# Performance work log

Hardware: AMD Instinct MI355X
Metric: run time of the kernel (lower is better)

## Reference

```python
import jax, jax.numpy as jnp
import numpy as np

B, S, D = 8, 2048, 1024  # batch, seq_len, emb_dim == qkv_dim
NEG = -999999.0  # module uses -999999 instead of -inf


def setup_inputs() -> dict:
    key = jax.random.key(0)
    ks = jax.random.split(key, 4)
    inputs = jax.random.normal(ks[0], (B, S, D), dtype=jnp.float32)
    # causal mask, flax attention layout [B, 1, S, S]
    causal = jnp.tril(jnp.ones((S, S), dtype=bool))
    mask = jnp.broadcast_to(causal, (B, 1, S, S))
    scale = 1.0 / np.sqrt(D)
    Wq = jax.random.normal(ks[1], (D, D), dtype=jnp.float32) * scale
    Wk = jax.random.normal(ks[2], (D, D), dtype=jnp.float32) * scale
    Wv = jax.random.normal(ks[3], (D, D), dtype=jnp.float32) * scale
    z = jnp.zeros((D,), dtype=jnp.float32)
    return {"inputs": inputs, "mask": mask, "Wq": Wq, "bq": z, "Wk": Wk,
            "bk": z, "Wv": Wv, "bv": z}


def reference(inputs, mask, Wq, bq, Wk, bk, Wv, bv):
    q = inputs @ Wq + bq  # [B,S,D]
    k = inputs @ Wk + bk
    v = inputs @ Wv + bv
    depth = q.shape[-1]
    q = q / jnp.sqrt(jnp.asarray(depth, q.dtype))
    attn = jnp.einsum('bqd,bkd->bqk', q, k)  # [B,S,S]
    attn = jnp.where(jnp.squeeze(mask, axis=1), attn, NEG)
    attn = jax.nn.softmax(attn, axis=-1)
    return attn @ v  # [B,S,D]
```

## Files before the change

### kernel.cpp

```cpp
#include <hip/hip_runtime.h>
#include <hip/hip_bf16.h>
#include <cstdint>

#define S_LEN 2048
#define D_DIM 1024
#define NB 8

typedef __attribute__((ext_vector_type(8))) short bf16x8;
typedef __attribute__((ext_vector_type(4))) float f32x4;

__device__ __forceinline__ unsigned short f2bf(float f) {
  union { float f; unsigned u; } x; x.f = f;
  unsigned r = x.u + 0x7fffu + ((x.u >> 16) & 1u);
  return (unsigned short)(r >> 16);
}
__device__ __forceinline__ void gload16(const void* g, void* l) {
  __builtin_amdgcn_global_load_lds((const __attribute__((address_space(1))) void*)g,
                                   (__attribute__((address_space(3))) void*)l, 16, 0, 0);
}

__global__ __launch_bounds__(256)
void cvt_f32_bf16(const float* __restrict__ in, unsigned short* __restrict__ out, int n4) {
  int i = blockIdx.x * blockDim.x + threadIdx.x;
  if (i >= n4) return;
  float4 v = reinterpret_cast<const float4*>(in)[i];
  ushort4 o;
  o.x = f2bf(v.x); o.y = f2bf(v.y); o.z = f2bf(v.z); o.w = f2bf(v.w);
  reinterpret_cast<ushort4*>(out)[i] = o;
}

__global__ __launch_bounds__(256)
void transpose_f32_bf16(const float* __restrict__ in, unsigned short* __restrict__ out,
                        int rows, int cols) {
  __shared__ unsigned short tile[32][33];
  int bx = blockIdx.x * 32, by = blockIdx.y * 32;
  int tx = threadIdx.x, ty = threadIdx.y;
  #pragma unroll
  for (int i = ty; i < 32; i += 8)
    tile[i][tx] = f2bf(in[(size_t)(by + i) * cols + bx + tx]);
  __syncthreads();
  #pragma unroll
  for (int i = ty; i < 32; i += 8)
    out[(size_t)(bx + i) * rows + by + tx] = tile[tx][i];
}

__global__ __launch_bounds__(256)
void transpose_bf16(const unsigned short* __restrict__ in, unsigned short* __restrict__ out,
                    int ldin, int ldout, long zin, long zout) {
  __shared__ unsigned short tile[32][33];
  const unsigned short* ip = in + (size_t)blockIdx.z * zin;
  unsigned short* op = out + (size_t)blockIdx.z * zout;
  int bx = blockIdx.x * 32, by = blockIdx.y * 32;
  int tx = threadIdx.x, ty = threadIdx.y;
  #pragma unroll
  for (int i = ty; i < 32; i += 8)
    tile[i][tx] = ip[(size_t)(by + i) * ldin + bx + tx];
  __syncthreads();
  #pragma unroll
  for (int i = ty; i < 32; i += 8)
    op[(size_t)(bx + i) * ldout + by + tx] = tile[tx][i];
}

#define LDFRAG(S, BUF, MH)                                                        \
  { _Pragma("unroll") for (int i_ = 0; i_ < 4; ++i_)                              \
      af##S[i_] = *reinterpret_cast<const bf16x8*>(&As[BUF][offA[(MH)*4+i_]]);    \
    _Pragma("unroll") for (int i_ = 0; i_ < 4; ++i_)                              \
      bf##S[i_] = *reinterpret_cast<const bf16x8*>(&Bs[BUF][offB[i_]]); }

#define DOMFMA(S, MH)                                                             \
  { __builtin_amdgcn_s_setprio(1);                                                \
    _Pragma("unroll") for (int i_ = 0; i_ < 4; ++i_)                              \
      _Pragma("unroll") for (int j_ = 0; j_ < 4; ++j_)                            \
        acc[(MH)*4+i_][j_] = __builtin_amdgcn_mfma_f32_16x16x32_bf16(             \
            af##S[i_], bf##S[j_], acc[(MH)*4+i_][j_], 0, 0, 0);                   \
    __builtin_amdgcn_s_setprio(0); }

template<int MODE>
__global__ __launch_bounds__(512, 2)
void gemm8(const unsigned short* __restrict__ Aall, const unsigned short* __restrict__ Btall,
           void* __restrict__ Call, int Kd, int lda, int ldb, int ldc,
           long sAz, long sBz, long sCz,
           const float* __restrict__ b0, const float* __restrict__ b1,
           const float* __restrict__ b2, float* __restrict__ rowsum, int ntn) {
  __shared__ __align__(16) unsigned short As[4][8192];
  __shared__ __align__(16) unsigned short Bs[4][8192];
  int nwg = gridDim.x, bid = blockIdx.x;
  int wg = (bid & 7) * (nwg >> 3) + (bid >> 3);
  int tm = wg / ntn, tn = wg % ntn;
  int z = blockIdx.z;
  if (MODE == 1 && tn > tm) return;
  const unsigned short* A  = Aall  + (size_t)z * sAz;
  const unsigned short* Bt = Btall + (size_t)z * sBz;
  int m0 = tm * 256, n0 = tn * 256;
  int t = threadIdx.x, lane = t & 63, w = t >> 6;
  int wr = w >> 2, wc = w & 3;
  int lr = lane & 15, lq = lane >> 4;
  int nkt = (MODE == 2) ? (tm + 1) * 8 : (Kd >> 5);

  int offA[8], offB[4];
  #pragma unroll
  for (int mi = 0; mi < 8; ++mi) {
    int row = wr * 128 + mi * 16 + lr;
    offA[mi] = row * 32 + ((lq ^ ((row >> 1) & 3)) * 8);
  }
  #pragma unroll
  for (int ni = 0; ni < 4; ++ni) {
    int row = wc * 64 + ni * 16 + lr;
    offB[ni] = row * 32 + ((lq ^ ((row >> 1) & 3)) * 8);
  }
  int srow[2], soff[2];
  #pragma unroll
  for (int c = 0; c < 2; ++c) {
    int r = c * 128 + w * 16 + (lane >> 2);
    srow[c] = r;
    soff[c] = ((lane & 3) ^ ((r >> 1) & 3)) * 8;
  }

  f32x4 acc[8][4];
  f32x4 zero4 = {0.f, 0.f, 0.f, 0.f};
  #pragma unroll
  for (int mi = 0; mi < 8; ++mi)
    #pragma unroll
    for (int ni = 0; ni < 4; ++ni) acc[mi][ni] = zero4;

  auto stgA = [&](int buf, int kt2) {
    int kb = kt2 * 32;
    #pragma unroll
    for (int c = 0; c < 2; ++c)
      gload16(A + (size_t)(m0 + srow[c]) * lda + kb + soff[c], &As[buf][c * 4096 + w * 512]);
  };
  auto stgB = [&](int buf, int kt2) {
    int kb = kt2 * 32;
    #pragma unroll
    for (int c = 0; c < 2; ++c)
      gload16(Bt + (size_t)(n0 + srow[c]) * ldb + kb + soff[c], &Bs[buf][c * 4096 + w * 512]);
  };

  stgA(0, 0); stgB(0, 0); stgA(1, 1); stgB(1, 1); stgA(2, 2); stgB(2, 2);
  asm volatile("s_waitcnt vmcnt(8)" ::: "memory");
  __builtin_amdgcn_s_barrier();
  __builtin_amdgcn_sched_barrier(0);
  bf16x8 af0[4], bf0[4], af1[4], bf1[4];
  LDFRAG(0, 0, 0);

  for (int kt = 0; kt < nkt; ++kt) {
    int bcur = kt & 3, bpre = (kt + 3) & 3, bnxt = (kt + 1) & 3;
    bool stg = (kt + 3 < nkt);
    if (stg) stgA(bpre, kt + 3);
    LDFRAG(1, bcur, 1);
    asm volatile("s_waitcnt lgkmcnt(8)" ::: "memory");
    __builtin_amdgcn_sched_barrier(0);
    DOMFMA(0, 0);
    if (stg) stgB(bpre, kt + 3);
    if (kt + 1 < nkt) {
      if (kt <= nkt - 4)      asm volatile("s_waitcnt vmcnt(8)" ::: "memory");
      else if (kt == nkt - 3) asm volatile("s_waitcnt vmcnt(4)" ::: "memory");
      else                    asm volatile("s_waitcnt vmcnt(0)" ::: "memory");
      __builtin_amdgcn_s_barrier();
      __builtin_amdgcn_sched_barrier(0);
      LDFRAG(0, bnxt, 0);
      asm volatile("s_waitcnt lgkmcnt(8)" ::: "memory");
    } else {
      asm volatile("s_waitcnt lgkmcnt(0)" ::: "memory");
    }
    __builtin_amdgcn_sched_barrier(0);
    DOMFMA(1, 1);
  }
  __syncthreads();

  unsigned short* ep = &As[0][0] + w * 4096;
  int lq4 = lq << 4;

  if (MODE == 0) {
    unsigned short* C = (unsigned short*)Call;
    #pragma unroll
    for (int mh = 0; mh < 2; ++mh) {
      #pragma unroll
      for (int mi2 = 0; mi2 < 4; ++mi2)
        #pragma unroll
        for (int ni = 0; ni < 4; ++ni) {
          int col = ni * 16 + lr;
          int gcol = n0 + wc * 64 + col;
          float bb, sc;
          if (gcol < 1024)      { bb = b0[gcol];        sc = 0.03125f; }
          else if (gcol < 2048) { bb = b1[gcol - 1024]; sc = 1.0f; }
          else                  { bb = b2[gcol - 2048]; sc = 1.0f; }
          #pragma unroll
          for (int j = 0; j < 4; ++j) {
            int lrow = mi2 * 16 + lq * 4 + j;
            ep[lrow * 64 + (col ^ lq4)] = f2bf((acc[mh * 4 + mi2][ni][j] + bb) * sc);
          }
        }
      #pragma unroll
      for (int pass = 0; pass < 8; ++pass) {
        int rrow = pass * 8 + (lane >> 3);
        int c8 = (lane & 7) * 8;
        int sw = ((rrow >> 2) & 3) << 4;
        bf16x8 vv = *reinterpret_cast<const bf16x8*>(&ep[rrow * 64 + (c8 ^ sw)]);
        int grow = m0 + wr * 128 + mh * 64 + rrow;
        *reinterpret_cast<bf16x8*>(&C[(size_t)grow * ldc + n0 + wc * 64 + c8]) = vv;
      }
      asm volatile("s_waitcnt lgkmcnt(0)" ::: "memory");
    }
  } else if (MODE == 1) {
    unsigned short* C = (unsigned short*)Call + (size_t)z * sCz;
    float* rs = rowsum + z * S_LEN;
    #pragma unroll
    for (int mh = 0; mh < 2; ++mh) {
      #pragma unroll
      for (int mi2 = 0; mi2 < 4; ++mi2)
        #pragma unroll
        for (int j = 0; j < 4; ++j) {
          int lrow = mi2 * 16 + lq * 4 + j;
          int grow = m0 + wr * 128 + mh * 64 + lrow;
          float partial = 0.f;
          #pragma unroll
          for (int ni = 0; ni < 4; ++ni) {
            int col = ni * 16 + lr;
            int gcol = n0 + wc * 64 + col;
            float e = (gcol <= grow) ? __expf(acc[mh * 4 + mi2][ni][j]) : 0.f;
            partial += e;
            ep[lrow * 64 + (col ^ lq4)] = f2bf(e);
          }
          #pragma unroll
          for (int off = 1; off < 16; off <<= 1) partial += __shfl_xor(partial, off);
          if (lr == 0) atomicAdd(&rs[grow], partial);
        }
      #pragma unroll
      for (int pass = 0; pass < 8; ++pass) {
        int rrow = pass * 8 + (lane >> 3);
        int c8 = (lane & 7) * 8;
        int sw = ((rrow >> 2) & 3) << 4;
        bf16x8 vv = *reinterpret_cast<const bf16x8*>(&ep[rrow * 64 + (c8 ^ sw)]);
        int grow = m0 + wr * 128 + mh * 64 + rrow;
        *reinterpret_cast<bf16x8*>(&C[(size_t)grow * ldc + n0 + wc * 64 + c8]) = vv;
      }
      asm volatile("s_waitcnt lgkmcnt(0)" ::: "memory");
    }
  } else {
    float* C = (float*)Call + (size_t)z * sCz;
    const float* rs = rowsum + z * S_LEN;
    #pragma unroll
    for (int mi = 0; mi < 8; ++mi)
      #pragma unroll
      for (int j = 0; j < 4; ++j) {
        int row = m0 + wr * 128 + mi * 16 + lq * 4 + j;
        float inv = 1.f / rs[row];
        #pragma unroll
        for (int ni = 0; ni < 4; ++ni) {
          int col = n0 + wc * 64 + ni * 16 + lr;
          C[(size_t)row * ldc + col] = acc[mi][ni][j] * inv;
        }
      }
  }
}

extern "C" void kernel_launch(void* const* d_in, const int* in_sizes, int n_in,
                              void* d_out, int out_size, void* d_ws, size_t ws_size,
                              hipStream_t stream) {
  (void)in_sizes; (void)n_in; (void)out_size; (void)ws_size;
  const float* X  = (const float*)d_in[0];
  const float* Wq = (const float*)d_in[2];
  const float* bq = (const float*)d_in[3];
  const float* Wk = (const float*)d_in[4];
  const float* bk = (const float*)d_in[5];
  const float* Wv = (const float*)d_in[6];
  const float* bv = (const float*)d_in[7];

  char* ws = (char*)d_ws;
  unsigned short* Xb  = (unsigned short*)(ws);
  unsigned short* Wt  = (unsigned short*)(ws + 33554432L);
  float*          Rs  = (float*)(ws + 33554432L);
  unsigned short* QKV = (unsigned short*)(ws + 39845888L);
  unsigned short* Pb  = (unsigned short*)(ws + 140509184L);
  unsigned short* Vt  = Xb;

  cvt_f32_bf16<<<16384, 256, 0, stream>>>(X, Xb, (NB * S_LEN * D_DIM) / 4);
  dim3 tb(32, 8);
  transpose_f32_bf16<<<dim3(32, 32), tb, 0, stream>>>(Wq, Wt + 0L * 1048576L, D_DIM, D_DIM);
  transpose_f32_bf16<<<dim3(32, 32), tb, 0, stream>>>(Wk, Wt + 1L * 1048576L, D_DIM, D_DIM);
  transpose_f32_bf16<<<dim3(32, 32), tb, 0, stream>>>(Wv, Wt + 2L * 1048576L, D_DIM, D_DIM);
  gemm8<0><<<dim3(64 * 12, 1, 1), 512, 0, stream>>>(Xb, Wt, (void*)QKV,
      D_DIM, D_DIM, D_DIM, 3 * D_DIM,
      0L, 0L, 0L, bq, bk, bv, nullptr, 12);
  hipMemsetAsync(Rs, 0, NB * S_LEN * sizeof(float), stream);
  gemm8<1><<<dim3(64, 1, NB), 512, 0, stream>>>(QKV, QKV + 1024, (void*)Pb,
      D_DIM, 3 * D_DIM, 3 * D_DIM, S_LEN,
      (long)S_LEN * 3 * D_DIM, (long)S_LEN * 3 * D_DIM, (long)S_LEN * S_LEN,
      nullptr, nullptr, nullptr, Rs, 8);
  transpose_bf16<<<dim3(32, 64, NB), tb, 0, stream>>>(QKV + 2048, Vt,
      3 * D_DIM, S_LEN, (long)S_LEN * 3 * D_DIM, (long)D_DIM * S_LEN);
  gemm8<2><<<dim3(32, 1, NB), 512, 0, stream>>>(Pb, Vt, d_out,
      S_LEN, S_LEN, S_LEN, D_DIM,
      (long)S_LEN * S_LEN, (long)D_DIM * S_LEN, (long)S_LEN * D_DIM,
      nullptr, nullptr, nullptr, Rs, 4);
}
```

Baseline: 340.1 us.

## Restructure GEMM main loop to two-stage prefetch with barrier-interleaved MFMA phases

Replaces the 3-deep global-to-LDS prefetch, which double-buffered register fragments across iterations, with a 2-deep prefetch. Each iteration now loads its A/B fragments, runs half the MFMAs, loads the second A half, and runs the other half. Extra s_barriers around each MFMA phase are meant to keep waves in lockstep, ping-ponging between memory and compute. The trade-off is that it drops the cross-iteration overlap of LDS reads with MFMAs and adds barriers. The shallower prefetch may also expose global-load latency.

```diff
diff --git a/kernel.cpp b/kernel.cpp
--- a/kernel.cpp
+++ b/kernel.cpp
@@ -60,20 +60,6 @@
   for (int i = ty; i < 32; i += 8)
     op[(size_t)(bx + i) * ldout + by + tx] = tile[tx][i];
 }
-
-#define LDFRAG(S, BUF, MH)                                                        \
-  { _Pragma("unroll") for (int i_ = 0; i_ < 4; ++i_)                              \
-      af##S[i_] = *reinterpret_cast<const bf16x8*>(&As[BUF][offA[(MH)*4+i_]]);    \
-    _Pragma("unroll") for (int i_ = 0; i_ < 4; ++i_)                              \
-      bf##S[i_] = *reinterpret_cast<const bf16x8*>(&Bs[BUF][offB[i_]]); }
-
-#define DOMFMA(S, MH)                                                             \
-  { __builtin_amdgcn_s_setprio(1);                                                \
-    _Pragma("unroll") for (int i_ = 0; i_ < 4; ++i_)                              \
-      _Pragma("unroll") for (int j_ = 0; j_ < 4; ++j_)                            \
-        acc[(MH)*4+i_][j_] = __builtin_amdgcn_mfma_f32_16x16x32_bf16(             \
-            af##S[i_], bf##S[j_], acc[(MH)*4+i_][j_], 0, 0, 0);                   \
-    __builtin_amdgcn_s_setprio(0); }
 
 template<int MODE>
 __global__ __launch_bounds__(512, 2)
@@ -136,35 +122,50 @@
       gload16(Bt + (size_t)(n0 + srow[c]) * ldb + kb + soff[c], &Bs[buf][c * 4096 + w * 512]);
   };
 
-  stgA(0, 0); stgB(0, 0); stgA(1, 1); stgB(1, 1); stgA(2, 2); stgB(2, 2);
-  asm volatile("s_waitcnt vmcnt(8)" ::: "memory");
+  stgA(0, 0); stgB(0, 0); stgA(1, 1); stgB(1, 1);
+  asm volatile("s_waitcnt vmcnt(4)" ::: "memory");
   __builtin_amdgcn_s_barrier();
-  __builtin_amdgcn_sched_barrier(0);
-  bf16x8 af0[4], bf0[4], af1[4], bf1[4];
-  LDFRAG(0, 0, 0);
 
   for (int kt = 0; kt < nkt; ++kt) {
-    int bcur = kt & 3, bpre = (kt + 3) & 3, bnxt = (kt + 1) & 3;
-    bool stg = (kt + 3 < nkt);
-    if (stg) stgA(bpre, kt + 3);
-    LDFRAG(1, bcur, 1);
-    asm volatile("s_waitcnt lgkmcnt(8)" ::: "memory");
+    const int bcur = kt & 3, bpre = (kt + 2) & 3;
+    const bool stg = (kt + 2 < nkt);
+    const unsigned short* Ac = &As[bcur][0];
+    const unsigned short* Bc = &Bs[bcur][0];
+    bf16x8 af[4], bfv[4];
+
+    #pragma unroll
+    for (int i = 0; i < 4; ++i) af[i]  = *reinterpret_cast<const bf16x8*>(&Ac[offA[i]]);
+    #pragma unroll
+    for (int i = 0; i < 4; ++i) bfv[i] = *reinterpret_cast<const bf16x8*>(&Bc[offB[i]]);
+    if (stg) stgA(bpre, kt + 2);
+    __builtin_amdgcn_s_barrier();
+    asm volatile("s_waitcnt lgkmcnt(0)" ::: "memory");
     __builtin_amdgcn_sched_barrier(0);
-    DOMFMA(0, 0);
-    if (stg) stgB(bpre, kt + 3);
-    if (kt + 1 < nkt) {
-      if (kt <= nkt - 4)      asm volatile("s_waitcnt vmcnt(8)" ::: "memory");
-      else if (kt == nkt - 3) asm volatile("s_waitcnt vmcnt(4)" ::: "memory");
-      else                    asm volatile("s_waitcnt vmcnt(0)" ::: "memory");
-      __builtin_amdgcn_s_barrier();
-      __builtin_amdgcn_sched_barrier(0);
-      LDFRAG(0, bnxt, 0);
-      asm volatile("s_waitcnt lgkmcnt(8)" ::: "memory");
-    } else {
-      asm volatile("s_waitcnt lgkmcnt(0)" ::: "memory");
-    }
+    __builtin_amdgcn_s_setprio(1);
+    #pragma unroll
+    for (int i = 0; i < 4; ++i)
+      #pragma unroll
+      for (int j = 0; j < 4; ++j)
+        acc[i][j] = __builtin_amdgcn_mfma_f32_16x16x32_bf16(af[i], bfv[j], acc[i][j], 0, 0, 0);
+    __builtin_amdgcn_s_setprio(0);
+    __builtin_amdgcn_s_barrier();
+
+    #pragma unroll
+    for (int i = 0; i < 4; ++i) af[i] = *reinterpret_cast<const bf16x8*>(&Ac[offA[4 + i]]);
+    if (stg) stgB(bpre, kt + 2);
+    if (kt + 2 < nkt)      asm volatile("s_waitcnt vmcnt(4)" ::: "memory");
+    else if (kt + 1 < nkt) asm volatile("s_waitcnt vmcnt(0)" ::: "memory");
+    __builtin_amdgcn_s_barrier();
+    asm volatile("s_waitcnt lgkmcnt(0)" ::: "memory");
     __builtin_amdgcn_sched_barrier(0);
-    DOMFMA(1, 1);
+    __builtin_amdgcn_s_setprio(1);
+    #pragma unroll
+    for (int i = 0; i < 4; ++i)
+      #pragma unroll
+      for (int j = 0; j < 4; ++j)
+        acc[4 + i][j] = __builtin_amdgcn_mfma_f32_16x16x32_bf16(af[i], bfv[j], acc[4 + i][j], 0, 0, 0);
+    __builtin_amdgcn_s_setprio(0);
+    __builtin_amdgcn_s_barrier();
   }
   __syncthreads();
 
```

Measured after the change: 328.0 us. 1.04x faster.
